# Kernel tuning notes

Measured on AMD Instinct MI355X. Metric: run time of the kernel, lower is better.

The kernel has to match this reference:

```python
import jax, jax.numpy as jnp
import numpy as np

NUM_CLASSES = 80
CONF_THRESH = 0.01
NMS_THRESH = 0.5
TOPK = 1000
LEVEL_SIZES = [230400, 57600, 14400]  # anchors per FPN level (img 3840, strides 8/16/32)
IMG_SIZE = 3840.0


def setup_inputs() -> dict:
    key = jax.random.key(0)
    inp = {}
    for l, M in enumerate(LEVEL_SIZES):
        kc, kctr, kwh = jax.random.split(jax.random.fold_in(key, l), 3)
        # classification logits; shift down so only a minority pass conf_thresh
        inp[f"cls_pred_{l}"] = jax.random.normal(kc, (1, M, NUM_CLASSES), jnp.float32) - 2.0
        # valid xyxy boxes: random centers + small w/h
        ctr = jax.random.uniform(kctr, (1, M, 2), jnp.float32) * IMG_SIZE
        wh = jax.random.uniform(kwh, (1, M, 2), jnp.float32) * 64.0 + 4.0
        inp[f"box_pred_{l}"] = jnp.concatenate([ctr - wh * 0.5, ctr + wh * 0.5], axis=-1)
    return inp


def _level_topk(cls_pred, box_pred):
    # cls_pred: [1, M, C], box_pred: [1, M, 4]  (multi-label path: flatten M*C)
    cls = cls_pred[0]
    box = box_pred[0]
    M, C = cls.shape
    scores_flat = jax.nn.sigmoid(cls).reshape(-1)            # [M*C]
    k = min(TOPK, M)
    topk_scores, topk_idxs = jax.lax.top_k(scores_flat, k)   # == sort desc + slice
    valid = topk_scores > CONF_THRESH                        # keep mask (padded, jit-safe)
    anchor_idxs = topk_idxs // C                             # label decode
    labels = topk_idxs % C
    bboxes = box[anchor_idxs]                                # [k, 4] gather
    return topk_scores, labels.astype(jnp.int32), bboxes, valid


def _pairwise_iou(boxes):
    # boxes: [N, 4] xyxy
    area = (boxes[:, 2] - boxes[:, 0]) * (boxes[:, 3] - boxes[:, 1])
    lt = jnp.maximum(boxes[:, None, :2], boxes[None, :, :2])
    rb = jnp.minimum(boxes[:, None, 2:], boxes[None, :, 2:])
    wh = jnp.clip(rb - lt, 0.0)
    inter = wh[..., 0] * wh[..., 1]
    union = area[:, None] + area[None, :] - inter
    return inter / jnp.maximum(union, 1e-9)


def _multiclass_nms(scores, labels, bboxes, valid, iou_thresh, class_agnostic=False):
    # Greedy NMS with fixed-size padded output (invalid entries get score 0 / label -1).
    N = scores.shape[0]
    scores = jnp.where(valid, scores, 0.0)
    order = jnp.argsort(-scores)
    scores, labels = scores[order], labels[order]
    bboxes, valid = bboxes[order], valid[order]
    if class_agnostic:
        nms_boxes = bboxes
    else:
        # batched-nms offset trick: boxes of different classes never overlap
        offset = labels.astype(bboxes.dtype)[:, None] * (jnp.max(bboxes) + 1.0)
        nms_boxes = bboxes + offset
    iou = _pairwise_iou(nms_boxes)  # [N, N]
    idx = jnp.arange(N)

    def body(i, keep):
        suppress = (iou[i] > iou_thresh) & keep[i] & (idx > i)
        return keep & (~suppress)

    keep = jax.lax.fori_loop(0, N, body, valid)
    out_scores = jnp.where(keep, scores, 0.0)
    out_labels = jnp.where(keep, labels, -1)
    out_bboxes = bboxes * keep[:, None].astype(bboxes.dtype)
    return out_bboxes, out_scores, out_labels


def reference(cls_pred_0, box_pred_0, cls_pred_1, box_pred_1, cls_pred_2, box_pred_2):
    cls_list = [cls_pred_0, cls_pred_1, cls_pred_2]
    box_list = [box_pred_0, box_pred_1, box_pred_2]
    all_s, all_l, all_b, all_v = [], [], [], []
    for c, b in zip(cls_list, box_list):
        s, l, bb, v = _level_topk(c, b)
        all_s.append(s); all_l.append(l); all_b.append(bb); all_v.append(v)
    scores = jnp.concatenate(all_s, 0)
    labels = jnp.concatenate(all_l, 0)
    bboxes = jnp.concatenate(all_b, 0)
    valid = jnp.concatenate(all_v, 0)
    bboxes, scores, labels = _multiclass_nms(scores, labels, bboxes, valid, NMS_THRESH)
    return bboxes, scores, labels
```

## Files before the change

### kernel.cpp

```cpp
#include <hip/hip_runtime.h>
#include <hip/hip_bf16.h>
#include <math.h>

typedef unsigned int u32;
typedef unsigned long long u64;
typedef unsigned char u8;

#define NBINS 8192
#define BIN_SHIFT 19
#define K_TOP 1000
#define NUM_C 80
#define N_ALL 3000
#define CAND_CAP 4096
#define PAIR_CAP 2048
#define IOU_TH 0.5f
#define CONF_TH 0.01f
#define FLOOR_KEY 0x80000000u
#define HIST_BASE 4096
#define NBINS_H   4096

#define L0_M 230400
#define L1_M 57600
#define L2_M 14400
#define L0_N (L0_M*NUM_C)
#define L1_N (L1_M*NUM_C)
#define L2_N (L2_M*NUM_C)
#define HB0 576
#define HB1 144
#define HB2 36
#define HBT (HB0+HB1+HB2)

#define RB_THREADS 64
#define RB_PER_LVL (CAND_CAP/RB_THREADS)

#define WS_HIST    0
#define WS_CTRL    98304
#define WS_CAND    98336
#define WS_PAIRS   196640
#define WS_SCORESA 213024
#define WS_LABELSA 225024
#define WS_VALIDA  237024
#define WS_BOXA    249024
#define WS_SSCORE  297024
#define WS_SLABEL  309024
#define WS_SVALID  321024
#define WS_SBOX    333024
#define WS_OBOX    381024

__device__ __forceinline__ u32 fkey(float f){
  u32 b = __float_as_uint(f);
  return (b & 0x80000000u) ? ~b : (b | 0x80000000u);
}
__device__ __forceinline__ float fdec(u32 e){
  u32 b = (e & 0x80000000u) ? (e ^ 0x80000000u) : ~e;
  return __uint_as_float(b);
}
__device__ __forceinline__ float ref_sigmoid(float x){
  return (float)(1.0 / (1.0 + exp(-(double)x)));
}

__device__ __forceinline__ void level_of_block(int b, const float* c0, const float* c1, const float* c2,
    int& level, const float4*& src, int& n4, int& lb, int& nb){
  if (b < HB0)            { level=0; src=(const float4*)c0; n4=L0_N/4; lb=b;          nb=HB0; }
  else if (b < HB0+HB1)   { level=1; src=(const float4*)c1; n4=L1_N/4; lb=b-HB0;      nb=HB1; }
  else                    { level=2; src=(const float4*)c2; n4=L2_N/4; lb=b-HB0-HB1;  nb=HB2; }
}

__global__ __launch_bounds__(256) void k_init(u32* ws32){
  int i = blockIdx.x*256 + threadIdx.x;
  if (i < 3*NBINS + 8) ws32[i] = 0;
}

__global__ __launch_bounds__(256) void k_hist(const float* __restrict__ c0, const float* __restrict__ c1,
                                              const float* __restrict__ c2, u32* __restrict__ hist){
  __shared__ u32 h[NBINS_H];
  for (int i = threadIdx.x; i < NBINS_H; i += 256) h[i] = 0;
  __syncthreads();
  int level, n4, lb, nb; const float4* src;
  level_of_block(blockIdx.x, c0, c1, c2, level, src, n4, lb, nb);
  for (int i = lb*256 + threadIdx.x; i < n4; i += nb*256){
    float4 v = src[i];
    u32 kx = fkey(v.x), ky = fkey(v.y), kz = fkey(v.z), kw = fkey(v.w);
    if (kx >= FLOOR_KEY) atomicAdd(&h[(kx >> BIN_SHIFT) - HIST_BASE], 1u);
    if (ky >= FLOOR_KEY) atomicAdd(&h[(ky >> BIN_SHIFT) - HIST_BASE], 1u);
    if (kz >= FLOOR_KEY) atomicAdd(&h[(kz >> BIN_SHIFT) - HIST_BASE], 1u);
    if (kw >= FLOOR_KEY) atomicAdd(&h[(kw >> BIN_SHIFT) - HIST_BASE], 1u);
  }
  __syncthreads();
  u32* gh = hist + level*NBINS + HIST_BASE;
  for (int i = threadIdx.x; i < NBINS_H; i += 256){
    u32 c = h[i];
    if (c) atomicAdd(&gh[i], c);
  }
}

__global__ __launch_bounds__(1024) void k_thresh(const u32* __restrict__ hist, u32* __restrict__ ctrl){
  __shared__ u32 sa[1024], sb[1024];
  int tid = threadIdx.x;
  const u32* h = hist + blockIdx.x*NBINS;
  u32 loc[8]; u32 s = 0;
  #pragma unroll
  for (int j = 0; j < 8; j++){ loc[j] = h[tid*8 + j]; s += loc[j]; }
  sa[tid] = s; __syncthreads();
  u32* cur = sa; u32* nxt = sb;
  for (int d = 1; d < 1024; d <<= 1){
    u32 v = cur[tid];
    if (tid + d < 1024) v += cur[tid + d];
    nxt[tid] = v;
    __syncthreads();
    u32* t2 = cur; cur = nxt; nxt = t2;
  }
  u32 se = cur[tid] - s;
  u32 prevS = se;
  #pragma unroll
  for (int j = 7; j >= 0; j--){
    u32 S = prevS + loc[j];
    if (S >= K_TOP && prevS < K_TOP){
      int bin = tid*8 + j;
      int tb = bin > 0 ? bin - 1 : 0;
      ctrl[blockIdx.x] = ((u32)tb) << BIN_SHIFT;
    }
    prevS = S;
  }
}

__global__ __launch_bounds__(256) void k_compact(const float* __restrict__ c0, const float* __restrict__ c1,
                                                 const float* __restrict__ c2, u32* __restrict__ ctrl,
                                                 u64* __restrict__ cand){
  int level, n4, lb, nb; const float4* src;
  level_of_block(blockIdx.x, c0, c1, c2, level, src, n4, lb, nb);
  u32 T = ctrl[level];
  u32* cnt = &ctrl[3 + level];
  u64* cd = cand + level*CAND_CAP;
  for (int i = lb*256 + threadIdx.x; i < n4; i += nb*256){
    float4 v = src[i];
    u32 base = (u32)i * 4u;
    float vv[4] = {v.x, v.y, v.z, v.w};
    #pragma unroll
    for (int t = 0; t < 4; t++){
      if (fkey(vv[t]) >= T){
        float s = ref_sigmoid(vv[t]);
        u32 p = atomicAdd(cnt, 1u);
        if (p < CAND_CAP)
          cd[p] = ((u64)__float_as_uint(s) << 32) | (u64)(0xFFFFFFFFu - (base + t));
      }
    }
  }
}

__global__ __launch_bounds__(RB_THREADS) void k_rank(const float* __restrict__ b0, const float* __restrict__ b1,
                                                     const float* __restrict__ b2, u32* __restrict__ ctrl,
                                                     const u64* __restrict__ cand,
                                                     float* __restrict__ scoresA, int* __restrict__ labelsA,
                                                     u32* __restrict__ validA, float* __restrict__ boxA){
  __shared__ u64 key[CAND_CAP];
  int level = blockIdx.x / RB_PER_LVL;
  int base  = (blockIdx.x % RB_PER_LVL) * RB_THREADS;
  int tid = threadIdx.x;
  u32 cnt = ctrl[3 + level]; if (cnt > CAND_CAP) cnt = CAND_CAP;
  int g = level*K_TOP + base + tid;
  if (base + tid >= (int)cnt && base + tid < K_TOP){
    scoresA[g] = 0.0f; labelsA[g] = 0; validA[g] = 0u;
    ((float4*)boxA)[g] = make_float4(0.f, 0.f, 0.f, 0.f);
  }
  if (base >= (int)cnt) return;
  int cntE = (int)((cnt + 1u) & ~1u);
  const u64* cd = cand + level*CAND_CAP;
  for (int i = tid; i < cntE; i += RB_THREADS)
    key[i] = (i < (int)cnt) ? cd[i] : 0ull;
  __syncthreads();
  int i = base + tid;
  u64 my = (i < (int)cnt) ? key[i] : ~0ull;
  int rk = 0;
  for (int j = 0; j < cntE; j += 2){
    ulonglong2 kk = *(const ulonglong2*)&key[j];
    rk += (kk.x > my) ? 1 : 0;
    rk += (kk.y > my) ? 1 : 0;
  }
  const float* bp = (level == 0) ? b0 : (level == 1 ? b1 : b2);
  u32 maxe = 0;
  if (i < (int)cnt && rk < K_TOP){
    float s = __uint_as_float((u32)(my >> 32));
    u32 idx = 0xFFFFFFFFu - (u32)my;
    int anchor = (int)(idx / NUM_C);
    int lab = (int)(idx - (u32)anchor*NUM_C);
    float4 bx = ((const float4*)bp)[anchor];
    int go = level*K_TOP + rk;
    scoresA[go] = s;
    labelsA[go] = lab;
    validA[go] = (s > CONF_TH) ? 1u : 0u;
    ((float4*)boxA)[go] = bx;
    maxe = max(max(fkey(bx.x), fkey(bx.y)), max(fkey(bx.z), fkey(bx.w)));
  }
  #pragma unroll
  for (int d = 32; d > 0; d >>= 1)
    maxe = max(maxe, (u32)__shfl_xor((int)maxe, d, 64));
  if (tid == 0 && maxe) atomicMax(&ctrl[6], maxe);
}

__global__ __launch_bounds__(1024) void k_merge(const u32* __restrict__ ctrl,
                                                const float* __restrict__ scoresA, const int* __restrict__ labelsA,
                                                const u32* __restrict__ validA, const float* __restrict__ boxA,
                                                float* __restrict__ sscore, int* __restrict__ slabel,
                                                u32* __restrict__ svalid, float* __restrict__ sbox,
                                                float* __restrict__ obox){
  #pragma clang fp contract(off)
  __shared__ float zs[N_ALL];
  int tid = threadIdx.x;
  for (int i = tid; i < N_ALL; i += 1024)
    zs[i] = validA[i] ? scoresA[i] : 0.0f;
  __syncthreads();
  float maxp1 = fdec(ctrl[6]) + 1.0f;
  for (int g = tid; g < N_ALL; g += 1024){
    int a = g / K_TOP;
    int p = g - a*K_TOP;
    float z = zs[g];
    int r = p;
    #pragma unroll
    for (int b = 0; b < 3; b++){
      if (b == a) continue;
      const float* arr = zs + b*K_TOP;
      int lo = 0, hi = K_TOP;
      if (b < a){
        while (lo < hi){ int mid = (lo + hi) >> 1; if (arr[mid] < z) hi = mid; else lo = mid + 1; }
      } else {
        while (lo < hi){ int mid = (lo + hi) >> 1; if (arr[mid] <= z) hi = mid; else lo = mid + 1; }
      }
      r += lo;
    }
    float4 bx = ((const float4*)boxA)[g];
    int lab = labelsA[g];
    sscore[r] = z;
    slabel[r] = lab;
    svalid[r] = validA[g];
    ((float4*)sbox)[r] = bx;
    float off = (float)lab * maxp1;
    float4 ob; ob.x = bx.x + off; ob.y = bx.y + off; ob.z = bx.z + off; ob.w = bx.w + off;
    ((float4*)obox)[r] = ob;
  }
}

__global__ __launch_bounds__(256) void k_pairs(const float* __restrict__ obox,
                                               u32* __restrict__ pairCnt, u64* __restrict__ pairs){
  #pragma clang fp contract(off)
  int i = blockIdx.x;
  const float4* ob = (const float4*)obox;
  float4 a = ob[i];
  float areaA = (a.z - a.x) * (a.w - a.y);
  for (int j = i + 1 + (int)threadIdx.x; j < N_ALL; j += 256){
    float4 b = ob[j];
    float areaB = (b.z - b.x) * (b.w - b.y);
    float ltx = fmaxf(a.x, b.x), lty = fmaxf(a.y, b.y);
    float rbx = fminf(a.z, b.z), rby = fminf(a.w, b.w);
    float w = fmaxf(rbx - ltx, 0.0f), h = fmaxf(rby - lty, 0.0f);
    float inter = w * h;
    float uni = (areaA + areaB) - inter;
    float iou = inter / fmaxf(uni, 1e-9f);
    if (iou > IOU_TH){
      u32 q = atomicAdd(pairCnt, 1u);
      if (q < PAIR_CAP) pairs[q] = ((u64)(u32)i << 32) | (u64)(u32)j;
    }
  }
}

__global__ __launch_bounds__(1024) void k_resolve(const u32* __restrict__ ctrl, const u64* __restrict__ pairs,
                                                  const float* __restrict__ sscore, const int* __restrict__ slabel,
                                                  const u32* __restrict__ svalid, const float* __restrict__ sbox,
                                                  float* __restrict__ out){
  __shared__ u64 pk[PAIR_CAP];
  __shared__ u8 keep[N_ALL];
  int tid = threadIdx.x;
  u32 P = ctrl[7]; if (P > PAIR_CAP) P = PAIR_CAP;
  for (int i = tid; i < (int)P; i += 1024) pk[i] = pairs[i];
  for (int i = tid; i < N_ALL; i += 1024) keep[i] = (u8)svalid[i];
  __syncthreads();
  u64 v0 = 0, v1 = 0; int r0 = -1, r1 = -1;
  if (tid < (int)P){ v0 = pk[tid]; r0 = 0; }
  if (tid + 1024 < (int)P){ v1 = pk[tid + 1024]; r1 = 0; }
  for (int j = 0; j < (int)P; j++){
    u64 pj = pk[j];
    if (r0 >= 0) r0 += (pj < v0) ? 1 : 0;
    if (r1 >= 0) r1 += (pj < v1) ? 1 : 0;
  }
  __syncthreads();
  if (r0 >= 0) pk[r0] = v0;
  if (r1 >= 0) pk[r1] = v1;
  __syncthreads();
  if (tid == 0){
    for (u32 e = 0; e < P; ++e){
      u64 k = pk[e];
      u32 i = (u32)(k >> 32), j = (u32)k;
      if (keep[i]) keep[j] = 0;
    }
  }
  __syncthreads();
  for (int r = tid; r < N_ALL; r += 1024){
    bool kp = keep[r] != 0;
    float4 bx = ((const float4*)sbox)[r];
    out[r*4 + 0] = kp ? bx.x : 0.0f;
    out[r*4 + 1] = kp ? bx.y : 0.0f;
    out[r*4 + 2] = kp ? bx.z : 0.0f;
    out[r*4 + 3] = kp ? bx.w : 0.0f;
    out[4*N_ALL + r] = kp ? sscore[r] : 0.0f;
    out[5*N_ALL + r] = kp ? (float)slabel[r] : -1.0f;
  }
}

extern "C" void kernel_launch(void* const* d_in, const int* in_sizes, int n_in,
                              void* d_out, int out_size, void* d_ws, size_t ws_size,
                              hipStream_t stream){
  const float* c0 = (const float*)d_in[0];
  const float* b0 = (const float*)d_in[1];
  const float* c1 = (const float*)d_in[2];
  const float* b1 = (const float*)d_in[3];
  const float* c2 = (const float*)d_in[4];
  const float* b2 = (const float*)d_in[5];
  char* ws = (char*)d_ws;
  u32* hist    = (u32*)(ws + WS_HIST);
  u32* ctrl    = (u32*)(ws + WS_CTRL);
  u64* cand    = (u64*)(ws + WS_CAND);
  u64* pairs   = (u64*)(ws + WS_PAIRS);
  float* scoresA = (float*)(ws + WS_SCORESA);
  int*   labelsA = (int*)(ws + WS_LABELSA);
  u32*   validA  = (u32*)(ws + WS_VALIDA);
  float* boxA    = (float*)(ws + WS_BOXA);
  float* sscore  = (float*)(ws + WS_SSCORE);
  int*   slabel  = (int*)(ws + WS_SLABEL);
  u32*   svalid  = (u32*)(ws + WS_SVALID);
  float* sbox    = (float*)(ws + WS_SBOX);
  float* obox    = (float*)(ws + WS_OBOX);
  float* out     = (float*)d_out;

  hipLaunchKernelGGL(k_init, dim3(97), dim3(256), 0, stream, (u32*)ws);
  hipLaunchKernelGGL(k_hist, dim3(HBT), dim3(256), 0, stream, c0, c1, c2, hist);
  hipLaunchKernelGGL(k_thresh, dim3(3), dim3(1024), 0, stream, hist, ctrl);
  hipLaunchKernelGGL(k_compact, dim3(HBT), dim3(256), 0, stream, c0, c1, c2, ctrl, cand);
  hipLaunchKernelGGL(k_rank, dim3(3*RB_PER_LVL), dim3(RB_THREADS), 0, stream, b0, b1, b2, ctrl, cand,
                     scoresA, labelsA, validA, boxA);
  hipLaunchKernelGGL(k_merge, dim3(1), dim3(1024), 0, stream, ctrl, scoresA, labelsA, validA, boxA,
                     sscore, slabel, svalid, sbox, obox);
  hipLaunchKernelGGL(k_pairs, dim3(N_ALL - 1), dim3(256), 0, stream, obox, &ctrl[7], pairs);
  hipLaunchKernelGGL(k_resolve, dim3(1), dim3(1024), 0, stream, ctrl, pairs,
                     sscore, slabel, svalid, sbox, out);
}
```

Baseline: 247.0 us.

## Fuse NMS pipeline into one cooperative kernel with chunk-max skip in compaction

Merges the eight separate kernels into a single cooperative-launch kernel that uses grid-wide syncs between stages, removing per-launch overhead and idle gaps between dependent stages. The histogram pass also records a per-64-float4 chunk maximum bin, so the compaction pass can skip reloading chunks that cannot reach the threshold. Pair IoU testing is spread over a flat triangular index across the whole grid, and the rank and merge stages are reshaped to fit 256-thread blocks. The costs are grid.sync latency, smaller block sizes for the serial merge and resolve stages, and the launch depending on 1008 blocks being co-resident.

```diff
diff --git a/kernel.cpp b/kernel.cpp
--- a/kernel.cpp
+++ b/kernel.cpp
@@ -1,12 +1,14 @@
 #include <hip/hip_runtime.h>
-#include <hip/hip_bf16.h>
+#include <hip/hip_cooperative_groups.h>
 #include <math.h>
+
+namespace cg = cooperative_groups;
 
 typedef unsigned int u32;
 typedef unsigned long long u64;
+typedef unsigned short u16;
 typedef unsigned char u8;
 
-#define NBINS 8192
 #define BIN_SHIFT 19
 #define K_TOP 1000
 #define NUM_C 80
@@ -19,33 +21,31 @@
 #define HIST_BASE 4096
 #define NBINS_H   4096
 
-#define L0_M 230400
-#define L1_M 57600
-#define L2_M 14400
-#define L0_N (L0_M*NUM_C)
-#define L1_N (L1_M*NUM_C)
-#define L2_N (L2_M*NUM_C)
-#define HB0 576
-#define HB1 144
-#define HB2 36
-#define HBT (HB0+HB1+HB2)
-
-#define RB_THREADS 64
-#define RB_PER_LVL (CAND_CAP/RB_THREADS)
+#define L0_N4 4608000
+#define L1_N4 1152000
+#define L2_N4 288000
+#define HB0 768
+#define HB1 192
+#define HB2 48
+#define GRID 1008
+#define CB0 0
+#define CB1 72000
+#define CB2 90000
 
 #define WS_HIST    0
-#define WS_CTRL    98304
-#define WS_CAND    98336
-#define WS_PAIRS   196640
-#define WS_SCORESA 213024
-#define WS_LABELSA 225024
-#define WS_VALIDA  237024
-#define WS_BOXA    249024
-#define WS_SSCORE  297024
-#define WS_SLABEL  309024
-#define WS_SVALID  321024
-#define WS_SBOX    333024
-#define WS_OBOX    381024
+#define WS_CTRL    49152
+#define WS_CAND    49184
+#define WS_PAIRS   147488
+#define WS_SCORESA 163872
+#define WS_LABELSA 175872
+#define WS_VALIDA  187872
+#define WS_BOXA    199872
+#define WS_SSCORE  247872
+#define WS_SLABEL  259872
+#define WS_SVALID  271872
+#define WS_SBOX    283872
+#define WS_OBOX    331872
+#define WS_CMAX    379872
 
 __device__ __forceinline__ u32 fkey(float f){
   u32 b = __float_as_uint(f);
@@ -58,251 +58,279 @@
 __device__ __forceinline__ float ref_sigmoid(float x){
   return (float)(1.0 / (1.0 + exp(-(double)x)));
 }
-
-__device__ __forceinline__ void level_of_block(int b, const float* c0, const float* c1, const float* c2,
-    int& level, const float4*& src, int& n4, int& lb, int& nb){
-  if (b < HB0)            { level=0; src=(const float4*)c0; n4=L0_N/4; lb=b;          nb=HB0; }
-  else if (b < HB0+HB1)   { level=1; src=(const float4*)c1; n4=L1_N/4; lb=b-HB0;      nb=HB1; }
-  else                    { level=2; src=(const float4*)c2; n4=L2_N/4; lb=b-HB0-HB1;  nb=HB2; }
-}
-
-__global__ __launch_bounds__(256) void k_init(u32* ws32){
-  int i = blockIdx.x*256 + threadIdx.x;
-  if (i < 3*NBINS + 8) ws32[i] = 0;
-}
-
-__global__ __launch_bounds__(256) void k_hist(const float* __restrict__ c0, const float* __restrict__ c1,
-                                              const float* __restrict__ c2, u32* __restrict__ hist){
-  __shared__ u32 h[NBINS_H];
-  for (int i = threadIdx.x; i < NBINS_H; i += 256) h[i] = 0;
-  __syncthreads();
-  int level, n4, lb, nb; const float4* src;
-  level_of_block(blockIdx.x, c0, c1, c2, level, src, n4, lb, nb);
-  for (int i = lb*256 + threadIdx.x; i < n4; i += nb*256){
-    float4 v = src[i];
-    u32 kx = fkey(v.x), ky = fkey(v.y), kz = fkey(v.z), kw = fkey(v.w);
-    if (kx >= FLOOR_KEY) atomicAdd(&h[(kx >> BIN_SHIFT) - HIST_BASE], 1u);
-    if (ky >= FLOOR_KEY) atomicAdd(&h[(ky >> BIN_SHIFT) - HIST_BASE], 1u);
-    if (kz >= FLOOR_KEY) atomicAdd(&h[(kz >> BIN_SHIFT) - HIST_BASE], 1u);
-    if (kw >= FLOOR_KEY) atomicAdd(&h[(kw >> BIN_SHIFT) - HIST_BASE], 1u);
-  }
-  __syncthreads();
-  u32* gh = hist + level*NBINS + HIST_BASE;
-  for (int i = threadIdx.x; i < NBINS_H; i += 256){
-    u32 c = h[i];
-    if (c) atomicAdd(&gh[i], c);
-  }
-}
-
-__global__ __launch_bounds__(1024) void k_thresh(const u32* __restrict__ hist, u32* __restrict__ ctrl){
-  __shared__ u32 sa[1024], sb[1024];
-  int tid = threadIdx.x;
-  const u32* h = hist + blockIdx.x*NBINS;
-  u32 loc[8]; u32 s = 0;
+__device__ __forceinline__ u64 ftri(int i){
+  return (u64)i * (u64)(2*N_ALL - 1 - i) / 2ull;
+}
+__device__ __forceinline__ u32 wavemax(u32 m, int tid){
   #pragma unroll
-  for (int j = 0; j < 8; j++){ loc[j] = h[tid*8 + j]; s += loc[j]; }
-  sa[tid] = s; __syncthreads();
-  u32* cur = sa; u32* nxt = sb;
-  for (int d = 1; d < 1024; d <<= 1){
-    u32 v = cur[tid];
-    if (tid + d < 1024) v += cur[tid + d];
-    nxt[tid] = v;
-    __syncthreads();
-    u32* t2 = cur; cur = nxt; nxt = t2;
-  }
-  u32 se = cur[tid] - s;
-  u32 prevS = se;
+  for (int d = 32; d > 0; d >>= 1){
+    u32 t = (u32)__shfl_xor((int)m, d, 64);
+    m = m > t ? m : t;
+  }
+  return m;
+}
+__device__ __forceinline__ void hist_acc(float4 v, int i, int tid, u32* h, u16* cm, int cbase){
+  u32 k0 = fkey(v.x), k1 = fkey(v.y), k2 = fkey(v.z), k3 = fkey(v.w);
+  if (k0 >= FLOOR_KEY) atomicAdd(&h[(k0 >> BIN_SHIFT) - HIST_BASE], 1u);
+  if (k1 >= FLOOR_KEY) atomicAdd(&h[(k1 >> BIN_SHIFT) - HIST_BASE], 1u);
+  if (k2 >= FLOOR_KEY) atomicAdd(&h[(k2 >> BIN_SHIFT) - HIST_BASE], 1u);
+  if (k3 >= FLOOR_KEY) atomicAdd(&h[(k3 >> BIN_SHIFT) - HIST_BASE], 1u);
+  u32 m = max(max(k0, k1), max(k2, k3));
+  m = wavemax(m, tid);
+  if ((tid & 63) == 0) cm[cbase + (i >> 6)] = (u16)(m >> BIN_SHIFT);
+}
+__device__ __forceinline__ void cand_test(float4 v, u32 base, u32 T, u32* cnt, u64* cd){
+  float vv[4] = {v.x, v.y, v.z, v.w};
   #pragma unroll
-  for (int j = 7; j >= 0; j--){
-    u32 S = prevS + loc[j];
-    if (S >= K_TOP && prevS < K_TOP){
-      int bin = tid*8 + j;
-      int tb = bin > 0 ? bin - 1 : 0;
-      ctrl[blockIdx.x] = ((u32)tb) << BIN_SHIFT;
-    }
-    prevS = S;
-  }
-}
-
-__global__ __launch_bounds__(256) void k_compact(const float* __restrict__ c0, const float* __restrict__ c1,
-                                                 const float* __restrict__ c2, u32* __restrict__ ctrl,
-                                                 u64* __restrict__ cand){
-  int level, n4, lb, nb; const float4* src;
-  level_of_block(blockIdx.x, c0, c1, c2, level, src, n4, lb, nb);
-  u32 T = ctrl[level];
-  u32* cnt = &ctrl[3 + level];
-  u64* cd = cand + level*CAND_CAP;
-  for (int i = lb*256 + threadIdx.x; i < n4; i += nb*256){
-    float4 v = src[i];
-    u32 base = (u32)i * 4u;
-    float vv[4] = {v.x, v.y, v.z, v.w};
+  for (int t = 0; t < 4; t++){
+    if (fkey(vv[t]) >= T){
+      float s = ref_sigmoid(vv[t]);
+      u32 p = atomicAdd(cnt, 1u);
+      if (p < CAND_CAP)
+        cd[p] = ((u64)__float_as_uint(s) << 32) | (u64)(0xFFFFFFFFu - (base + t));
+    }
+  }
+}
+
+__global__ __launch_bounds__(256, 4) void k_fused(
+    const float* __restrict__ c0, const float* __restrict__ b0,
+    const float* __restrict__ c1, const float* __restrict__ b1,
+    const float* __restrict__ c2, const float* __restrict__ b2,
+    u32* __restrict__ hist, u32* __restrict__ ctrl, u64* __restrict__ cand,
+    u16* __restrict__ cmax,
+    float* __restrict__ scoresA, int* __restrict__ labelsA, u32* __restrict__ validA,
+    float* __restrict__ boxA,
+    float* __restrict__ sscore, int* __restrict__ slabel, u32* __restrict__ svalid,
+    float* __restrict__ sbox, float* __restrict__ obox,
+    u64* __restrict__ pairsBuf, float* __restrict__ out)
+{
+  #pragma clang fp contract(off)
+  cg::grid_group grid = cg::this_grid();
+  const int tid = threadIdx.x;
+  const int blk = blockIdx.x;
+  const int gt  = blk*256 + tid;
+  __shared__ __align__(16) u8 smem[19456];
+
+  if (gt < 3*NBINS_H + 8) hist[gt] = 0;
+  grid.sync();
+
+  int level, lb, nb, n4, cbase; const float4* src;
+  if (blk < HB0)            { level=0; lb=blk;          nb=HB0; n4=L0_N4; src=(const float4*)c0; cbase=CB0; }
+  else if (blk < HB0+HB1)   { level=1; lb=blk-HB0;      nb=HB1; n4=L1_N4; src=(const float4*)c1; cbase=CB1; }
+  else                      { level=2; lb=blk-HB0-HB1;  nb=HB2; n4=L2_N4; src=(const float4*)c2; cbase=CB2; }
+  const int lstr = nb*256;
+
+  {
+    u32* h = (u32*)smem;
+    for (int i = tid; i < NBINS_H; i += 256) h[i] = 0;
+    __syncthreads();
+    int i = lb*256 + tid;
+    for (; i + lstr < n4; i += 2*lstr){
+      float4 va = src[i];
+      float4 vb = src[i + lstr];
+      hist_acc(va, i, tid, h, cmax, cbase);
+      hist_acc(vb, i + lstr, tid, h, cmax, cbase);
+    }
+    if (i < n4){
+      float4 va = src[i];
+      hist_acc(va, i, tid, h, cmax, cbase);
+    }
+    __syncthreads();
+    u32* gh = hist + level*NBINS_H;
+    for (int i2 = tid; i2 < NBINS_H; i2 += 256){
+      u32 c = h[i2];
+      if (c) atomicAdd(&gh[i2], c);
+    }
+  }
+  grid.sync();
+
+  if (blk < 3){
+    u32* sa = (u32*)smem;
+    u32* sb = sa + 256;
+    const u32* hh = hist + blk*NBINS_H;
+    u32 loc[16]; u32 s = 0;
     #pragma unroll
-    for (int t = 0; t < 4; t++){
-      if (fkey(vv[t]) >= T){
-        float s = ref_sigmoid(vv[t]);
-        u32 p = atomicAdd(cnt, 1u);
-        if (p < CAND_CAP)
-          cd[p] = ((u64)__float_as_uint(s) << 32) | (u64)(0xFFFFFFFFu - (base + t));
-      }
-    }
-  }
-}
-
-__global__ __launch_bounds__(RB_THREADS) void k_rank(const float* __restrict__ b0, const float* __restrict__ b1,
-                                                     const float* __restrict__ b2, u32* __restrict__ ctrl,
-                                                     const u64* __restrict__ cand,
-                                                     float* __restrict__ scoresA, int* __restrict__ labelsA,
-                                                     u32* __restrict__ validA, float* __restrict__ boxA){
-  __shared__ u64 key[CAND_CAP];
-  int level = blockIdx.x / RB_PER_LVL;
-  int base  = (blockIdx.x % RB_PER_LVL) * RB_THREADS;
-  int tid = threadIdx.x;
-  u32 cnt = ctrl[3 + level]; if (cnt > CAND_CAP) cnt = CAND_CAP;
-  int g = level*K_TOP + base + tid;
-  if (base + tid >= (int)cnt && base + tid < K_TOP){
-    scoresA[g] = 0.0f; labelsA[g] = 0; validA[g] = 0u;
-    ((float4*)boxA)[g] = make_float4(0.f, 0.f, 0.f, 0.f);
-  }
-  if (base >= (int)cnt) return;
-  int cntE = (int)((cnt + 1u) & ~1u);
-  const u64* cd = cand + level*CAND_CAP;
-  for (int i = tid; i < cntE; i += RB_THREADS)
-    key[i] = (i < (int)cnt) ? cd[i] : 0ull;
-  __syncthreads();
-  int i = base + tid;
-  u64 my = (i < (int)cnt) ? key[i] : ~0ull;
-  int rk = 0;
-  for (int j = 0; j < cntE; j += 2){
-    ulonglong2 kk = *(const ulonglong2*)&key[j];
-    rk += (kk.x > my) ? 1 : 0;
-    rk += (kk.y > my) ? 1 : 0;
-  }
-  const float* bp = (level == 0) ? b0 : (level == 1 ? b1 : b2);
-  u32 maxe = 0;
-  if (i < (int)cnt && rk < K_TOP){
-    float s = __uint_as_float((u32)(my >> 32));
-    u32 idx = 0xFFFFFFFFu - (u32)my;
-    int anchor = (int)(idx / NUM_C);
-    int lab = (int)(idx - (u32)anchor*NUM_C);
-    float4 bx = ((const float4*)bp)[anchor];
-    int go = level*K_TOP + rk;
-    scoresA[go] = s;
-    labelsA[go] = lab;
-    validA[go] = (s > CONF_TH) ? 1u : 0u;
-    ((float4*)boxA)[go] = bx;
-    maxe = max(max(fkey(bx.x), fkey(bx.y)), max(fkey(bx.z), fkey(bx.w)));
-  }
-  #pragma unroll
-  for (int d = 32; d > 0; d >>= 1)
-    maxe = max(maxe, (u32)__shfl_xor((int)maxe, d, 64));
-  if (tid == 0 && maxe) atomicMax(&ctrl[6], maxe);
-}
-
-__global__ __launch_bounds__(1024) void k_merge(const u32* __restrict__ ctrl,
-                                                const float* __restrict__ scoresA, const int* __restrict__ labelsA,
-                                                const u32* __restrict__ validA, const float* __restrict__ boxA,
-                                                float* __restrict__ sscore, int* __restrict__ slabel,
-                                                u32* __restrict__ svalid, float* __restrict__ sbox,
-                                                float* __restrict__ obox){
-  #pragma clang fp contract(off)
-  __shared__ float zs[N_ALL];
-  int tid = threadIdx.x;
-  for (int i = tid; i < N_ALL; i += 1024)
-    zs[i] = validA[i] ? scoresA[i] : 0.0f;
-  __syncthreads();
-  float maxp1 = fdec(ctrl[6]) + 1.0f;
-  for (int g = tid; g < N_ALL; g += 1024){
-    int a = g / K_TOP;
-    int p = g - a*K_TOP;
-    float z = zs[g];
-    int r = p;
-    #pragma unroll
-    for (int b = 0; b < 3; b++){
-      if (b == a) continue;
-      const float* arr = zs + b*K_TOP;
-      int lo = 0, hi = K_TOP;
-      if (b < a){
-        while (lo < hi){ int mid = (lo + hi) >> 1; if (arr[mid] < z) hi = mid; else lo = mid + 1; }
-      } else {
-        while (lo < hi){ int mid = (lo + hi) >> 1; if (arr[mid] <= z) hi = mid; else lo = mid + 1; }
-      }
-      r += lo;
-    }
-    float4 bx = ((const float4*)boxA)[g];
-    int lab = labelsA[g];
-    sscore[r] = z;
-    slabel[r] = lab;
-    svalid[r] = validA[g];
-    ((float4*)sbox)[r] = bx;
-    float off = (float)lab * maxp1;
-    float4 ob; ob.x = bx.x + off; ob.y = bx.y + off; ob.z = bx.z + off; ob.w = bx.w + off;
-    ((float4*)obox)[r] = ob;
-  }
-}
-
-__global__ __launch_bounds__(256) void k_pairs(const float* __restrict__ obox,
-                                               u32* __restrict__ pairCnt, u64* __restrict__ pairs){
-  #pragma clang fp contract(off)
-  int i = blockIdx.x;
-  const float4* ob = (const float4*)obox;
-  float4 a = ob[i];
-  float areaA = (a.z - a.x) * (a.w - a.y);
-  for (int j = i + 1 + (int)threadIdx.x; j < N_ALL; j += 256){
-    float4 b = ob[j];
-    float areaB = (b.z - b.x) * (b.w - b.y);
-    float ltx = fmaxf(a.x, b.x), lty = fmaxf(a.y, b.y);
-    float rbx = fminf(a.z, b.z), rby = fminf(a.w, b.w);
-    float w = fmaxf(rbx - ltx, 0.0f), h = fmaxf(rby - lty, 0.0f);
-    float inter = w * h;
-    float uni = (areaA + areaB) - inter;
-    float iou = inter / fmaxf(uni, 1e-9f);
-    if (iou > IOU_TH){
-      u32 q = atomicAdd(pairCnt, 1u);
-      if (q < PAIR_CAP) pairs[q] = ((u64)(u32)i << 32) | (u64)(u32)j;
-    }
-  }
-}
-
-__global__ __launch_bounds__(1024) void k_resolve(const u32* __restrict__ ctrl, const u64* __restrict__ pairs,
-                                                  const float* __restrict__ sscore, const int* __restrict__ slabel,
-                                                  const u32* __restrict__ svalid, const float* __restrict__ sbox,
-                                                  float* __restrict__ out){
-  __shared__ u64 pk[PAIR_CAP];
-  __shared__ u8 keep[N_ALL];
-  int tid = threadIdx.x;
-  u32 P = ctrl[7]; if (P > PAIR_CAP) P = PAIR_CAP;
-  for (int i = tid; i < (int)P; i += 1024) pk[i] = pairs[i];
-  for (int i = tid; i < N_ALL; i += 1024) keep[i] = (u8)svalid[i];
-  __syncthreads();
-  u64 v0 = 0, v1 = 0; int r0 = -1, r1 = -1;
-  if (tid < (int)P){ v0 = pk[tid]; r0 = 0; }
-  if (tid + 1024 < (int)P){ v1 = pk[tid + 1024]; r1 = 0; }
-  for (int j = 0; j < (int)P; j++){
-    u64 pj = pk[j];
-    if (r0 >= 0) r0 += (pj < v0) ? 1 : 0;
-    if (r1 >= 0) r1 += (pj < v1) ? 1 : 0;
-  }
-  __syncthreads();
-  if (r0 >= 0) pk[r0] = v0;
-  if (r1 >= 0) pk[r1] = v1;
-  __syncthreads();
-  if (tid == 0){
-    for (u32 e = 0; e < P; ++e){
-      u64 k = pk[e];
-      u32 i = (u32)(k >> 32), j = (u32)k;
-      if (keep[i]) keep[j] = 0;
-    }
-  }
-  __syncthreads();
-  for (int r = tid; r < N_ALL; r += 1024){
-    bool kp = keep[r] != 0;
-    float4 bx = ((const float4*)sbox)[r];
-    out[r*4 + 0] = kp ? bx.x : 0.0f;
-    out[r*4 + 1] = kp ? bx.y : 0.0f;
-    out[r*4 + 2] = kp ? bx.z : 0.0f;
-    out[r*4 + 3] = kp ? bx.w : 0.0f;
-    out[4*N_ALL + r] = kp ? sscore[r] : 0.0f;
-    out[5*N_ALL + r] = kp ? (float)slabel[r] : -1.0f;
+    for (int j = 0; j < 16; j++){ loc[j] = hh[tid*16 + j]; s += loc[j]; }
+    sa[tid] = s; __syncthreads();
+    u32 *cur = sa, *nxt = sb;
+    for (int d = 1; d < 256; d <<= 1){
+      u32 v = cur[tid];
+      if (tid + d < 256) v += cur[tid + d];
+      nxt[tid] = v; __syncthreads();
+      u32* t2 = cur; cur = nxt; nxt = t2;
+    }
+    u32 prevS = cur[tid] - s;
+    for (int j = 15; j >= 0; j--){
+      u32 S = prevS + loc[j];
+      if (S >= K_TOP && prevS < K_TOP){
+        int binAbs = HIST_BASE + tid*16 + j;
+        ctrl[blk] = ((u32)(binAbs - 1)) << BIN_SHIFT;
+      }
+      prevS = S;
+    }
+  }
+  grid.sync();
+
+  {
+    const u32 T = ctrl[level];
+    const u32 B = T >> BIN_SHIFT;
+    u32* cnt = &ctrl[3 + level];
+    u64* cd = cand + level*CAND_CAP;
+    int i = lb*256 + tid;
+    for (; i + lstr < n4; i += 2*lstr){
+      u32 ca = cmax[cbase + (i >> 6)];
+      u32 cb = cmax[cbase + ((i + lstr) >> 6)];
+      if (ca >= B){ float4 v = src[i];        cand_test(v, (u32)i*4u,        T, cnt, cd); }
+      if (cb >= B){ float4 v = src[i + lstr]; cand_test(v, (u32)(i+lstr)*4u, T, cnt, cd); }
+    }
+    if (i < n4){
+      u32 ca = cmax[cbase + (i >> 6)];
+      if (ca >= B){ float4 v = src[i]; cand_test(v, (u32)i*4u, T, cnt, cd); }
+    }
+  }
+  grid.sync();
+
+  if (blk < 48){
+    int rl = blk >> 4;
+    int rb = (blk & 15) * 256;
+    u32 cnt = ctrl[3 + rl]; if (cnt > CAND_CAP) cnt = CAND_CAP;
+    const u64* cd = cand + rl*CAND_CAP;
+    const float* bp = (rl == 0) ? b0 : (rl == 1 ? b1 : b2);
+    int slot = rb + tid;
+    if (slot >= (int)cnt && slot < K_TOP){
+      int g = rl*K_TOP + slot;
+      scoresA[g] = 0.f; labelsA[g] = 0; validA[g] = 0u;
+      ((float4*)boxA)[g] = make_float4(0.f, 0.f, 0.f, 0.f);
+    }
+    if (rb < (int)cnt){
+      u64* keys = (u64*)smem;
+      u64 my = (slot < (int)cnt) ? cd[slot] : ~0ull;
+      int rk = 0;
+      for (u32 hb = 0; hb < cnt; hb += 2048){
+        u32 m = cnt - hb; if (m > 2048) m = 2048;
+        u32 mE = (m + 1u) & ~1u;
+        __syncthreads();
+        for (u32 t = tid; t < mE; t += 256)
+          keys[t] = (hb + t < cnt) ? cd[hb + t] : 0ull;
+        __syncthreads();
+        for (u32 j = 0; j < mE; j += 2){
+          ulonglong2 kk = *(const ulonglong2*)&keys[j];
+          rk += (kk.x > my) ? 1 : 0;
+          rk += (kk.y > my) ? 1 : 0;
+        }
+      }
+      u32 maxe = 0;
+      if (slot < (int)cnt && rk < K_TOP){
+        float s = __uint_as_float((u32)(my >> 32));
+        u32 idx = 0xFFFFFFFFu - (u32)my;
+        int anchor = (int)(idx / NUM_C);
+        int lab = (int)(idx - (u32)anchor*NUM_C);
+        float4 bx = ((const float4*)bp)[anchor];
+        int go = rl*K_TOP + rk;
+        scoresA[go] = s; labelsA[go] = lab;
+        validA[go] = (s > CONF_TH) ? 1u : 0u;
+        ((float4*)boxA)[go] = bx;
+        maxe = max(max(fkey(bx.x), fkey(bx.y)), max(fkey(bx.z), fkey(bx.w)));
+      }
+      maxe = wavemax(maxe, tid);
+      if ((tid & 63) == 0 && maxe) atomicMax(&ctrl[6], maxe);
+    }
+  }
+  grid.sync();
+
+  if (blk < 12){
+    float* zs = (float*)smem;
+    for (int i = tid; i < N_ALL; i += 256)
+      zs[i] = validA[i] ? scoresA[i] : 0.0f;
+    __syncthreads();
+    float maxp1 = fdec(ctrl[6]) + 1.0f;
+    int g = blk*256 + tid;
+    if (g < N_ALL){
+      int a = g / K_TOP;
+      int p = g - a*K_TOP;
+      float z = zs[g];
+      int r = p;
+      #pragma unroll
+      for (int b = 0; b < 3; b++){
+        if (b == a) continue;
+        const float* arr = zs + b*K_TOP;
+        int lo = 0, hi = K_TOP;
+        if (b < a){ while (lo < hi){ int mid=(lo+hi)>>1; if (arr[mid] <  z) hi=mid; else lo=mid+1; } }
+        else      { while (lo < hi){ int mid=(lo+hi)>>1; if (arr[mid] <= z) hi=mid; else lo=mid+1; } }
+        r += lo;
+      }
+      float4 bx = ((const float4*)boxA)[g];
+      int lab = labelsA[g];
+      sscore[r] = z; slabel[r] = lab; svalid[r] = validA[g];
+      ((float4*)sbox)[r] = bx;
+      float off = (float)lab * maxp1;
+      float4 ob; ob.x = bx.x+off; ob.y = bx.y+off; ob.z = bx.z+off; ob.w = bx.w+off;
+      ((float4*)obox)[r] = ob;
+    }
+  }
+  grid.sync();
+
+  {
+    const float4* ob = (const float4*)obox;
+    const u64 PT = (u64)N_ALL*(N_ALL-1)/2;
+    for (u64 p = (u64)gt; p < PT; p += (u64)(GRID*256)){
+      double disc = 5999.0*5999.0 - 8.0*(double)p;
+      int i = (int)((5999.0 - sqrt(disc)) * 0.5);
+      if (i < 0) i = 0; if (i > N_ALL-2) i = N_ALL-2;
+      while (ftri(i+1) <= p) ++i;
+      while (ftri(i) > p) --i;
+      int j = i + 1 + (int)(p - ftri(i));
+      float4 a = ob[i], b = ob[j];
+      float areaA = (a.z - a.x) * (a.w - a.y);
+      float areaB = (b.z - b.x) * (b.w - b.y);
+      float ltx = fmaxf(a.x, b.x), lty = fmaxf(a.y, b.y);
+      float rbx = fminf(a.z, b.z), rby = fminf(a.w, b.w);
+      float w = fmaxf(rbx - ltx, 0.0f), h = fmaxf(rby - lty, 0.0f);
+      float inter = w * h;
+      float uni = (areaA + areaB) - inter;
+      float iou = inter / fmaxf(uni, 1e-9f);
+      if (iou > IOU_TH){
+        u32 q = atomicAdd(&ctrl[7], 1u);
+        if (q < PAIR_CAP) pairsBuf[q] = ((u64)(u32)i << 32) | (u64)(u32)j;
+      }
+    }
+  }
+  grid.sync();
+
+  if (blk == 0){
+    u64* pk  = (u64*)smem;
+    u8* keep = smem + 16384;
+    u32 P = ctrl[7]; if (P > PAIR_CAP) P = PAIR_CAP;
+    for (int i = tid; i < (int)P; i += 256) pk[i] = pairsBuf[i];
+    for (int i = tid; i < N_ALL; i += 256) keep[i] = (u8)svalid[i];
+    __syncthreads();
+    u64 val[8]; int rr[8]; int ns = 0;
+    for (int s = tid; s < (int)P; s += 256){ val[ns] = pk[s]; rr[ns] = 0; ns++; }
+    for (int j = 0; j < (int)P; j++){
+      u64 pj = pk[j];
+      for (int q = 0; q < ns; q++) rr[q] += (pj < val[q]) ? 1 : 0;
+    }
+    __syncthreads();
+    for (int q = 0; q < ns; q++) pk[rr[q]] = val[q];
+    __syncthreads();
+    if (tid == 0){
+      for (u32 e = 0; e < P; ++e){
+        u64 k = pk[e];
+        u32 i = (u32)(k >> 32), j = (u32)k;
+        if (keep[i]) keep[j] = 0;
+      }
+    }
+    __syncthreads();
+    for (int r = tid; r < N_ALL; r += 256){
+      bool kp = keep[r] != 0;
+      float4 bx = ((const float4*)sbox)[r];
+      out[r*4 + 0] = kp ? bx.x : 0.0f;
+      out[r*4 + 1] = kp ? bx.y : 0.0f;
+      out[r*4 + 2] = kp ? bx.z : 0.0f;
+      out[r*4 + 3] = kp ? bx.w : 0.0f;
+      out[4*N_ALL + r] = kp ? sscore[r] : 0.0f;
+      out[5*N_ALL + r] = kp ? (float)slabel[r] : -1.0f;
+    }
   }
 }
 
@@ -316,10 +344,10 @@
   const float* c2 = (const float*)d_in[4];
   const float* b2 = (const float*)d_in[5];
   char* ws = (char*)d_ws;
-  u32* hist    = (u32*)(ws + WS_HIST);
-  u32* ctrl    = (u32*)(ws + WS_CTRL);
-  u64* cand    = (u64*)(ws + WS_CAND);
-  u64* pairs   = (u64*)(ws + WS_PAIRS);
+  u32* hist     = (u32*)(ws + WS_HIST);
+  u32* ctrl     = (u32*)(ws + WS_CTRL);
+  u64* cand     = (u64*)(ws + WS_CAND);
+  u64* pairsBuf = (u64*)(ws + WS_PAIRS);
   float* scoresA = (float*)(ws + WS_SCORESA);
   int*   labelsA = (int*)(ws + WS_LABELSA);
   u32*   validA  = (u32*)(ws + WS_VALIDA);
@@ -329,17 +357,14 @@
   u32*   svalid  = (u32*)(ws + WS_SVALID);
   float* sbox    = (float*)(ws + WS_SBOX);
   float* obox    = (float*)(ws + WS_OBOX);
-  float* out     = (float*)d_out;
-
-  hipLaunchKernelGGL(k_init, dim3(97), dim3(256), 0, stream, (u32*)ws);
-  hipLaunchKernelGGL(k_hist, dim3(HBT), dim3(256), 0, stream, c0, c1, c2, hist);
-  hipLaunchKernelGGL(k_thresh, dim3(3), dim3(1024), 0, stream, hist, ctrl);
-  hipLaunchKernelGGL(k_compact, dim3(HBT), dim3(256), 0, stream, c0, c1, c2, ctrl, cand);
-  hipLaunchKernelGGL(k_rank, dim3(3*RB_PER_LVL), dim3(RB_THREADS), 0, stream, b0, b1, b2, ctrl, cand,
-                     scoresA, labelsA, validA, boxA);
-  hipLaunchKernelGGL(k_merge, dim3(1), dim3(1024), 0, stream, ctrl, scoresA, labelsA, validA, boxA,
-                     sscore, slabel, svalid, sbox, obox);
-  hipLaunchKernelGGL(k_pairs, dim3(N_ALL - 1), dim3(256), 0, stream, obox, &ctrl[7], pairs);
-  hipLaunchKernelGGL(k_resolve, dim3(1), dim3(1024), 0, stream, ctrl, pairs,
-                     sscore, slabel, svalid, sbox, out);
-}
+  u16*   cmaxp   = (u16*)(ws + WS_CMAX);
+  float* outp    = (float*)d_out;
+
+  void* args[] = { &c0, &b0, &c1, &b1, &c2, &b2,
+                   &hist, &ctrl, &cand, &cmaxp,
+                   &scoresA, &labelsA, &validA, &boxA,
+                   &sscore, &slabel, &svalid, &sbox, &obox,
+                   &pairsBuf, &outp };
+  hipLaunchCooperativeKernel((const void*)k_fused, dim3(GRID), dim3(256),
+                             args, 0, stream);
+}
```

After: 902.8 us. 3.65x slower.
